# Kernel tuning notes

Hardware: AMD Instinct MI355X
Metric: run time of the kernel (lower is better)

Reference implementation:

```python
import jax, jax.numpy as jnp
import numpy as np

MAX_ITERS = 50
EPS_NORM = 1e-8
EPS_SEP = -1e-6


def setup_inputs() -> dict:
    key = jax.random.key(0)
    k1, k2 = jax.random.split(key)
    pointcloud = jax.random.normal(k1, (200000, 3), dtype=jnp.float32)
    targets = jax.random.normal(k2, (256, 3), dtype=jnp.float32)
    return {"pointcloud": pointcloud, "targets": targets}


def reference(pointcloud, targets):
    # pointcloud: [N, d], targets: [M, d]
    N = pointcloud.shape[0]
    M = targets.shape[0]
    p2 = jnp.sum(pointcloud * pointcloud, axis=1)  # [N]
    t2 = jnp.sum(targets * targets, axis=1)        # [M]

    def step(mask, _):
        # squared euclidean distances [M, N] (argmin identical to cdist argmin)
        d2 = t2[:, None] + p2[None, :] - 2.0 * (targets @ pointcloud.T)
        d2 = jnp.where(mask, d2, jnp.inf)
        closest_idx = jnp.argmin(d2, axis=1)           # [M]
        closest_points = pointcloud[closest_idx]       # [M, d]
        a = closest_points - targets
        a = a / (jnp.linalg.norm(a, axis=1, keepdims=True) + EPS_NORM)
        b = jnp.sum(a * closest_points, axis=1)        # [M]
        dot = a @ pointcloud.T - b[:, None]            # [M, N]
        separated = dot >= EPS_SEP
        mask = mask & ~separated
        return mask, (a, b)

    mask0 = jnp.ones((M, N), dtype=bool)
    _, (a_stack, b_stack) = jax.lax.scan(step, mask0, None, length=MAX_ITERS)
    return a_stack, b_stack  # [MAX_ITERS, M, d], [MAX_ITERS, M]
```

## Files before the change

kernel.cpp:

```cpp
#include <hip/hip_runtime.h>
#include <stdint.h>
#include <math.h>

#pragma clang fp contract(off)

#define BLOCK 1024
#define NW 16
#define PT 8
#define MAX_ITERS 50
#define SOLO_CAP 2048
#define NBINS 4096
#define EPS_NORM 1e-8f
#define EPS_SEP (-1e-6f)
#define SLACK_ABS 1e-3f
#define SLACK_REL 1e-5f

__device__ __forceinline__ int bin_of(float x, float y, float z) {
    int cx = (int)floorf((x + 3.5f) * (16.0f / 7.0f));
    int cy = (int)floorf((y + 3.5f) * (16.0f / 7.0f));
    int cz = (int)floorf((z + 3.5f) * (16.0f / 7.0f));
    cx = cx < 0 ? 0 : (cx > 15 ? 15 : cx);
    cy = cy < 0 ? 0 : (cy > 15 ? 15 : cy);
    cz = cz < 0 ? 0 : (cz > 15 ? 15 : cz);
    int code = 0;
    #pragma unroll
    for (int b = 0; b < 4; ++b) {
        code |= ((cx >> b) & 1) << (3 * b);
        code |= ((cy >> b) & 1) << (3 * b + 1);
        code |= ((cz >> b) & 1) << (3 * b + 2);
    }
    return code;
}

__global__ void hist_bins(const float* __restrict__ pc, int* __restrict__ binCnt,
                          int N) {
    const int t = blockIdx.x * blockDim.x + threadIdx.x;
    const int base = t * 4;
    if (base + 3 < N) {
        const float4* p4 = (const float4*)pc;
        const float4 a = p4[3*t+0], b = p4[3*t+1], c = p4[3*t+2];
        atomicAdd(&binCnt[bin_of(a.x, a.y, a.z)], 1);
        atomicAdd(&binCnt[bin_of(a.w, b.x, b.y)], 1);
        atomicAdd(&binCnt[bin_of(b.z, b.w, c.x)], 1);
        atomicAdd(&binCnt[bin_of(c.y, c.z, c.w)], 1);
    } else {
        for (int i = base; i < N; ++i)
            atomicAdd(&binCnt[bin_of(pc[3*i], pc[3*i+1], pc[3*i+2])], 1);
    }
}

__global__ void scan_bins(const int* __restrict__ binCnt,
                          int* __restrict__ binCur) {
    __shared__ int wsum[16];
    const int t = threadIdx.x, lane = t & 63, wv = t >> 6;
    const int v0 = binCnt[4*t+0], v1 = binCnt[4*t+1],
              v2 = binCnt[4*t+2], v3 = binCnt[4*t+3];
    const int s = v0 + v1 + v2 + v3;
    int incl = s;
    #pragma unroll
    for (int off = 1; off < 64; off <<= 1) {
        int o = __shfl_up(incl, off, 64);
        if (lane >= off) incl += o;
    }
    if (lane == 63) wsum[wv] = incl;
    __syncthreads();
    if (t == 0) {
        int acc = 0;
        for (int w = 0; w < 16; ++w) { int x = wsum[w]; wsum[w] = acc; acc += x; }
    }
    __syncthreads();
    const int excl = incl - s + wsum[wv];
    binCur[4*t+0] = excl;
    binCur[4*t+1] = excl + v0;
    binCur[4*t+2] = excl + v0 + v1;
    binCur[4*t+3] = excl + v0 + v1 + v2;
}

__global__ void scatter_bins(const float* __restrict__ pc,
                             float4* __restrict__ pk,
                             int* __restrict__ binCur, int N) {
    const int t = blockIdx.x * blockDim.x + threadIdx.x;
    const int base = t * 4;
    if (base + 3 < N) {
        const float4* p4 = (const float4*)pc;
        const float4 a = p4[3*t+0], b = p4[3*t+1], c = p4[3*t+2];
        float x[4] = {a.x, a.w, b.z, c.y};
        float y[4] = {a.y, b.x, b.w, c.z};
        float z[4] = {a.z, b.y, c.x, c.w};
        #pragma unroll
        for (int q = 0; q < 4; ++q) {
            const int pos = atomicAdd(&binCur[bin_of(x[q], y[q], z[q])], 1);
            float4 v; v.x = x[q]; v.y = y[q]; v.z = z[q];
            v.w = __int_as_float(base + q);
            pk[pos] = v;
        }
    } else {
        for (int i = base; i < N; ++i) {
            const float xx = pc[3*i], yy = pc[3*i+1], zz = pc[3*i+2];
            const int pos = atomicAdd(&binCur[bin_of(xx, yy, zz)], 1);
            float4 v; v.x = xx; v.y = yy; v.z = zz; v.w = __int_as_float(i);
            pk[pos] = v;
        }
    }
}

__global__ void pack_identity(const float* __restrict__ pc,
                              float4* __restrict__ pk, int N) {
    const int i = blockIdx.x * blockDim.x + threadIdx.x;
    if (i < N) {
        float4 v; v.x = pc[3*i+0]; v.y = pc[3*i+1]; v.z = pc[3*i+2];
        v.w = __int_as_float(i);
        pk[i] = v;
    }
}

template <bool PK>
__global__ __launch_bounds__(BLOCK) void convex_plane_kernel(
    const float* __restrict__ pc, const float4* __restrict__ pk,
    const float* __restrict__ tg,
    float* __restrict__ out, int N, int M, int stepsA)
{
    extern __shared__ uint32_t smem[];
    const int tid  = threadIdx.x;
    const int lane = tid & 63;
    const int wv   = tid >> 6;
    const int m    = blockIdx.x;

    const int NC    = stepsA * NW;
    const int maskW = stepsA * (PT * BLOCK / 32);
    uint32_t* mask = smem;
    float* mnx = (float*)(mask + maskW);
    float* mny = mnx + NC;
    float* mnz = mny + NC;
    float* mxx = mnz + NC;
    float* mxy = mxx + NC;
    float* mxz = mxy + NC;
    float* cdm = mxz + NC;
    int*   cim = (int*)(cdm + NC);
    int*   ccn = cim + NC;
    float* red_d = (float*)(ccn + NC);
    int*   red_i = (int*)(red_d + NW);
    int*   cw    = red_i + NW;
    int*   bcast = cw + NW;
    int*   cnt   = bcast + 2;
    int*   slist = cnt + 1;
    float* lx = (float*)(slist + SOLO_CAP);
    float* ly = lx + SOLO_CAP;
    float* lz = ly + SOLO_CAP;

    const float tx = tg[3*m+0], ty = tg[3*m+1], tz = tg[3*m+2];
    const float t2 = tx*tx + ty*ty + tz*tz;

    float* out_a = out;
    float* out_b = out + (size_t)MAX_ITERS * (size_t)M * 3;

    auto ld8 = [&](int pbase, float px[PT], float py[PT], float pz[PT],
                   int ov[PT]) {
        #pragma unroll
        for (int j = 0; j < PT; ++j) {
            int ip = pbase + j * 64;
            ip = ip < N ? ip : N - 1;
            if constexpr (PK) {
                const float4 v = pk[ip];
                px[j] = v.x; py[j] = v.y; pz[j] = v.z;
                ov[j] = __float_as_int(v.w);
            } else {
                const float* p = pc + 3 * (size_t)ip;
                px[j] = p[0]; py[j] = p[1]; pz[j] = p[2];
                ov[j] = ip;
            }
        }
    };

    auto finish = [&]() -> int2 {
        __syncthreads();
        float bd = INFINITY; int bi = 0; int cs = 0;
        for (int l = lane; l < stepsA; l += 64) {
            const int c = wv + NW * l;
            const float d = cdm[c]; const int i = cim[c];
            if (d < bd || (d == bd && i < bi)) { bd = d; bi = i; }
            cs += ccn[c];
        }
        #pragma unroll
        for (int off = 32; off > 0; off >>= 1) {
            float od = __shfl_down(bd, off, 64);
            int   oi = __shfl_down(bi, off, 64);
            int   oc = __shfl_down(cs, off, 64);
            if (od < bd || (od == bd && oi < bi)) { bd = od; bi = oi; }
            cs += oc;
        }
        if (lane == 0) { red_d[wv] = bd; red_i[wv] = bi; cw[wv] = cs; }
        __syncthreads();
        if (wv == 0) {
            float d = (lane < NW) ? red_d[lane] : INFINITY;
            int   i = (lane < NW) ? red_i[lane] : 0;
            int   c = (lane < NW) ? cw[lane]    : 0;
            #pragma unroll
            for (int off = 8; off > 0; off >>= 1) {
                float od = __shfl_down(d, off, 64);
                int   oi = __shfl_down(i, off, 64);
                int   oc = __shfl_down(c, off, 64);
                if (od < d || (od == d && oi < i)) { d = od; i = oi; }
                c += oc;
            }
            if (lane == 0) { bcast[0] = i; bcast[1] = c; }
        }
        __syncthreads();
        int2 r; r.x = bcast[0]; r.y = bcast[1];
        return r;
    };

    auto writeChunk = [&](int c, uint32_t keepm,
                          float dmin, int imin,
                          float px[PT], float py[PT], float pz[PT]) {
        float nx = INFINITY, ny = INFINITY, nz = INFINITY;
        float Xx = -INFINITY, Xy = -INFINITY, Xz = -INFINITY;
        #pragma unroll
        for (int j = 0; j < PT; ++j) {
            if ((keepm >> j) & 1u) {
                nx = fminf(nx, px[j]); ny = fminf(ny, py[j]); nz = fminf(nz, pz[j]);
                Xx = fmaxf(Xx, px[j]); Xy = fmaxf(Xy, py[j]); Xz = fmaxf(Xz, pz[j]);
            }
        }
        int cntl = (int)__popc(keepm);
        #pragma unroll
        for (int off = 32; off > 0; off >>= 1) {
            float od = __shfl_down(dmin, off, 64);
            int   oi = __shfl_down(imin, off, 64);
            if (od < dmin || (od == dmin && oi < imin)) { dmin = od; imin = oi; }
            cntl += __shfl_down(cntl, off, 64);
            nx = fminf(nx, __shfl_down(nx, off, 64));
            ny = fminf(ny, __shfl_down(ny, off, 64));
            nz = fminf(nz, __shfl_down(nz, off, 64));
            Xx = fmaxf(Xx, __shfl_down(Xx, off, 64));
            Xy = fmaxf(Xy, __shfl_down(Xy, off, 64));
            Xz = fmaxf(Xz, __shfl_down(Xz, off, 64));
        }
        if (lane == 0) {
            cdm[c] = dmin; cim[c] = imin; ccn[c] = cntl;
            mnx[c] = nx; mny[c] = ny; mnz[c] = nz;
            mxx[c] = Xx; mxy[c] = Xy; mxz[c] = Xz;
        }
    };

    auto initScan = [&]() {
        for (int s = 0; s < stepsA; ++s) {
            const int c = s * NW + wv;
            const int pbase = s * (PT * BLOCK) + wv * (PT * 64) + lane;
            const int wwb   = s * (PT * BLOCK / 32) + wv * (PT * 2);
            uint32_t livem = 0;
            #pragma unroll
            for (int j = 0; j < PT; ++j)
                if (pbase + j * 64 < N) livem |= (1u << j);
            float px[PT], py[PT], pz[PT]; int ov[PT];
            ld8(pbase, px, py, pz, ov);
            float dmin = INFINITY; int imin = 0;
            #pragma unroll
            for (int j = 0; j < PT; ++j) {
                if ((livem >> j) & 1u) {
                    float p2 = px[j]*px[j] + py[j]*py[j] + pz[j]*pz[j];
                    float tp = tx*px[j] + ty*py[j] + tz*pz[j];
                    float d2 = t2 + p2 - 2.0f*tp;
                    if (d2 < dmin || (d2 == dmin && ov[j] < imin)) {
                        dmin = d2; imin = ov[j];
                    }
                }
            }
            #pragma unroll
            for (int j = 0; j < PT; ++j) {
                unsigned long long bal = __ballot(((livem >> j) & 1u) != 0u);
                if (lane == 0)       mask[wwb + j*2]     = (uint32_t)bal;
                else if (lane == 32) mask[wwb + j*2 + 1] = (uint32_t)(bal >> 32);
            }
            writeChunk(c, livem, dmin, imin, px, py, pz);
        }
    };

    auto stepScan = [&](float ax, float ay, float az, float b) {
        for (int s = 0; s < stepsA; ++s) {
            const int c = s * NW + wv;
            if (ccn[c] == 0) continue;
            const float ubx = fmaxf(ax*mnx[c], ax*mxx[c]);
            const float uby = fmaxf(ay*mny[c], ay*mxy[c]);
            const float ubz = fmaxf(az*mnz[c], az*mxz[c]);
            const float ub  = (ubx + uby + ubz) - b;
            const float sl  = SLACK_ABS + SLACK_REL * (fabsf(ub) + fabsf(b));
            if (ub < EPS_SEP - sl) continue;
            const float lbx = fminf(ax*mnx[c], ax*mxx[c]);
            const float lby = fminf(ay*mny[c], ay*mxy[c]);
            const float lbz = fminf(az*mnz[c], az*mxz[c]);
            const float lb  = (lbx + lby + lbz) - b;
            const float sl2 = SLACK_ABS + SLACK_REL * (fabsf(lb) + fabsf(b));
            if (lb >= EPS_SEP + sl2) {
                if (lane == 0) { ccn[c] = 0; cdm[c] = INFINITY; }
                continue;
            }
            const int pbase = s * (PT * BLOCK) + wv * (PT * 64) + lane;
            const int wwb   = s * (PT * BLOCK / 32) + wv * (PT * 2);
            uint32_t livem = 0;
            #pragma unroll
            for (int j = 0; j < PT; ++j) {
                uint32_t w = mask[wwb + j * 2 + (lane >> 5)];
                livem |= ((w >> (lane & 31)) & 1u) << j;
            }
            float px[PT], py[PT], pz[PT]; int ov[PT];
            ld8(pbase, px, py, pz, ov);
            uint32_t keepm = 0;
            float dmin = INFINITY; int imin = 0;
            #pragma unroll
            for (int j = 0; j < PT; ++j) {
                if ((livem >> j) & 1u) {
                    float dt = ax*px[j] + ay*py[j] + az*pz[j] - b;
                    if (dt < EPS_SEP) {
                        keepm |= (1u << j);
                        float p2 = px[j]*px[j] + py[j]*py[j] + pz[j]*pz[j];
                        float tp = tx*px[j] + ty*py[j] + tz*pz[j];
                        float d2 = t2 + p2 - 2.0f*tp;
                        if (d2 < dmin || (d2 == dmin && ov[j] < imin)) {
                            dmin = d2; imin = ov[j];
                        }
                    }
                }
            }
            #pragma unroll
            for (int j = 0; j < PT; ++j) {
                unsigned long long bal = __ballot(((keepm >> j) & 1u) != 0u);
                if (lane == 0)       mask[wwb + j*2]     = (uint32_t)bal;
                else if (lane == 32) mask[wwb + j*2 + 1] = (uint32_t)(bal >> 32);
            }
            writeChunk(c, keepm, dmin, imin, px, py, pz);
        }
    };

    initScan();
    int2 rc = finish();
    int idx = rc.x, count = rc.y;

    for (int k = 0; k < MAX_ITERS; ++k) {
        if (count <= SOLO_CAP && count > 0) {
            if (tid == 0) cnt[0] = 0;
            __syncthreads();
            for (int s = 0; s < stepsA; ++s) {
                const int c = s * NW + wv;
                if (ccn[c] == 0) continue;
                const int pbase = s * (PT * BLOCK) + wv * (PT * 64) + lane;
                const int wwb   = s * (PT * BLOCK / 32) + wv * (PT * 2);
                uint32_t livem = 0;
                #pragma unroll
                for (int j = 0; j < PT; ++j) {
                    uint32_t w = mask[wwb + j * 2 + (lane >> 5)];
                    livem |= ((w >> (lane & 31)) & 1u) << j;
                }
                float px[PT], py[PT], pz[PT]; int ov[PT];
                ld8(pbase, px, py, pz, ov);
                int cl = (int)__popc(livem);
                int incl = cl;
                #pragma unroll
                for (int off = 1; off < 64; off <<= 1) {
                    int o = __shfl_up(incl, off, 64);
                    if (lane >= off) incl += o;
                }
                const int excl = incl - cl;
                const int tot  = __shfl(incl, 63, 64);
                int wb = 0;
                if (lane == 0) wb = atomicAdd(cnt, tot);
                wb = __shfl(wb, 0, 64);
                int pos = wb + excl;
                #pragma unroll
                for (int j = 0; j < PT; ++j) {
                    if ((livem >> j) & 1u) {
                        slist[pos] = ov[j];
                        lx[pos] = px[j]; ly[pos] = py[j]; lz[pos] = pz[j];
                        ++pos;
                    }
                }
            }
            __syncthreads();
            if (wv != 0) return;
            for (; k < MAX_ITERS; ++k) {
                const float* cp = pc + 3 * (size_t)idx;
                const float cx = cp[0], cy = cp[1], cz = cp[2];
                const float vx = cx - tx, vy = cy - ty, vz = cz - tz;
                const float nrm = sqrtf(vx*vx + vy*vy + vz*vz);
                const float den = nrm + EPS_NORM;
                const float ax = vx / den, ay = vy / den, az = vz / den;
                const float b  = ax*cx + ay*cy + az*cz;
                if (count == 0) {
                    for (int q = lane; q < MAX_ITERS - k; q += 64) {
                        const int kk = k + q;
                        const size_t oa = ((size_t)kk * M + m) * 3;
                        out_a[oa+0] = ax; out_a[oa+1] = ay; out_a[oa+2] = az;
                        out_b[(size_t)kk * M + m] = b;
                    }
                    return;
                }
                if (lane == 0) {
                    const size_t oa = ((size_t)k * M + m) * 3;
                    out_a[oa+0] = ax; out_a[oa+1] = ay; out_a[oa+2] = az;
                    out_b[(size_t)k * M + m] = b;
                }
                if (k + 1 < MAX_ITERS) {
                    float dmin = INFINITY; int imin = 0; int wcur = 0;
                    for (int e0 = 0; e0 < count; e0 += 64) {
                        const int e = e0 + lane;
                        bool keep = false; int j = 0;
                        float d2v = 0.f, px = 0.f, py = 0.f, pz = 0.f;
                        if (e < count) {
                            j = slist[e];
                            px = lx[e]; py = ly[e]; pz = lz[e];
                            float dt = ax*px + ay*py + az*pz - b;
                            if (dt < EPS_SEP) {
                                keep = true;
                                float p2 = px*px + py*py + pz*pz;
                                float tp = tx*px + ty*py + tz*pz;
                                d2v = t2 + p2 - 2.0f*tp;
                            }
                        }
                        unsigned long long bal = __ballot(keep);
                        int pos = wcur + (int)__popcll(bal & ((1ull << lane) - 1ull));
                        if (keep) {
                            slist[pos] = j;
                            lx[pos] = px; ly[pos] = py; lz[pos] = pz;
                            if (d2v < dmin || (d2v == dmin && j < imin)) {
                                dmin = d2v; imin = j;
                            }
                        }
                        wcur += (int)__popcll(bal);
                    }
                    #pragma unroll
                    for (int off = 32; off > 0; off >>= 1) {
                        float od = __shfl_down(dmin, off, 64);
                        int   oi = __shfl_down(imin, off, 64);
                        if (od < dmin || (od == dmin && oi < imin)) { dmin = od; imin = oi; }
                    }
                    idx = __shfl(imin, 0, 64);
                    count = wcur;
                }
            }
            return;
        }

        const float* cp = pc + 3 * (size_t)idx;
        const float cx = cp[0], cy = cp[1], cz = cp[2];
        const float vx = cx - tx, vy = cy - ty, vz = cz - tz;
        const float nrm = sqrtf(vx*vx + vy*vy + vz*vz);
        const float den = nrm + EPS_NORM;
        const float ax = vx / den, ay = vy / den, az = vz / den;
        const float b  = ax*cx + ay*cy + az*cz;

        if (count == 0) {
            for (int q = tid; q < MAX_ITERS - k; q += BLOCK) {
                const int kk = k + q;
                const size_t oa = ((size_t)kk * M + m) * 3;
                out_a[oa+0] = ax; out_a[oa+1] = ay; out_a[oa+2] = az;
                out_b[(size_t)kk * M + m] = b;
            }
            return;
        }
        if (tid == 0) {
            const size_t oa = ((size_t)k * M + m) * 3;
            out_a[oa+0] = ax; out_a[oa+1] = ay; out_a[oa+2] = az;
            out_b[(size_t)k * M + m] = b;
        }
        if (k + 1 < MAX_ITERS) {
            stepScan(ax, ay, az, b);
            rc = finish();
            idx = rc.x; count = rc.y;
        }
    }
}

extern "C" void kernel_launch(void* const* d_in, const int* in_sizes, int n_in,
                              void* d_out, int out_size, void* d_ws, size_t ws_size,
                              hipStream_t stream) {
    const float* pc = (const float*)d_in[0];
    const float* tg = (const float*)d_in[1];
    float* out = (float*)d_out;
    const int N = in_sizes[0] / 3;
    const int M = in_sizes[1] / 3;
    const int stepsA = (N + BLOCK * PT - 1) / (BLOCK * PT);
    const int NC     = stepsA * NW;
    const int maskW  = stepsA * (PT * BLOCK / 32);
    const size_t smemW = (size_t)maskW + 9u * NC + 3u * NW + 3u
                       + 4u * SOLO_CAP;
    const size_t smem  = smemW * sizeof(uint32_t);
    const size_t pkB   = (size_t)N * sizeof(float4);
    const size_t binB  = 2 * (size_t)NBINS * sizeof(int);

    int wsmode = 0;
    if (d_ws && ws_size >= pkB + binB) wsmode = 2;
    else if (d_ws && ws_size >= pkB)   wsmode = 1;
    float4* pk     = (float4*)d_ws;
    int*    binCnt = (int*)((char*)d_ws + pkB);
    int*    binCur = binCnt + NBINS;

    hipFuncSetAttribute((const void*)convex_plane_kernel<true>,
                        hipFuncAttributeMaxDynamicSharedMemorySize, (int)smem);
    hipFuncSetAttribute((const void*)convex_plane_kernel<false>,
                        hipFuncAttributeMaxDynamicSharedMemorySize, (int)smem);

    if (wsmode == 2) {
        const int tpb = 256;
        const int vthreads = (N + 3) / 4;
        hipMemsetAsync(binCnt, 0, NBINS * sizeof(int), stream);
        hist_bins<<<(vthreads + tpb - 1) / tpb, tpb, 0, stream>>>(pc, binCnt, N);
        scan_bins<<<1, 1024, 0, stream>>>(binCnt, binCur);
        scatter_bins<<<(vthreads + tpb - 1) / tpb, tpb, 0, stream>>>(pc, pk,
                                                                     binCur, N);
        convex_plane_kernel<true><<<M, BLOCK, smem, stream>>>(
            pc, pk, tg, out, N, M, stepsA);
    } else if (wsmode == 1) {
        pack_identity<<<(N + 255) / 256, 256, 0, stream>>>(pc, pk, N);
        convex_plane_kernel<true><<<M, BLOCK, smem, stream>>>(
            pc, pk, tg, out, N, M, stepsA);
    } else {
        convex_plane_kernel<false><<<M, BLOCK, smem, stream>>>(
            pc, nullptr, tg, out, N, M, stepsA);
    }
}
```

Baseline: 572.6 us.

## Refine bounding-box culling to 64-point groups with quantized boxes and compacted work list

Culling now works on per-wavefront 64-point groups instead of 512-point chunks. Each group's bounding box is stored as 16-bit quantized coordinates, which keeps the per-group shared-memory state small. Each iteration first classifies all groups in parallel and compacts only the ambiguous ones into a list, which the wavefronts then process two at a time. The spatial binning grid also goes from 16^3 to 32^3 Morton cells so that groups are tighter. The aim is to load far fewer points per iteration, at the cost of a longer classification pass, more atomics and a scan kernel that walks 32 bins per thread serially.

```diff
diff --git a/kernel.cpp b/kernel.cpp
--- a/kernel.cpp
+++ b/kernel.cpp
@@ -6,25 +6,25 @@
 
 #define BLOCK 1024
 #define NW 16
-#define PT 8
 #define MAX_ITERS 50
 #define SOLO_CAP 2048
-#define NBINS 4096
+#define NBINS 32768
 #define EPS_NORM 1e-8f
 #define EPS_SEP (-1e-6f)
-#define SLACK_ABS 1e-3f
-#define SLACK_REL 1e-5f
+#define SLACK 1e-3f
+#define QSC 2048.0f
+#define QIN (1.0f/2048.0f)
 
 __device__ __forceinline__ int bin_of(float x, float y, float z) {
-    int cx = (int)floorf((x + 3.5f) * (16.0f / 7.0f));
-    int cy = (int)floorf((y + 3.5f) * (16.0f / 7.0f));
-    int cz = (int)floorf((z + 3.5f) * (16.0f / 7.0f));
-    cx = cx < 0 ? 0 : (cx > 15 ? 15 : cx);
-    cy = cy < 0 ? 0 : (cy > 15 ? 15 : cy);
-    cz = cz < 0 ? 0 : (cz > 15 ? 15 : cz);
+    int cx = (int)floorf((x + 3.5f) * (32.0f / 7.0f));
+    int cy = (int)floorf((y + 3.5f) * (32.0f / 7.0f));
+    int cz = (int)floorf((z + 3.5f) * (32.0f / 7.0f));
+    cx = cx < 0 ? 0 : (cx > 31 ? 31 : cx);
+    cy = cy < 0 ? 0 : (cy > 31 ? 31 : cy);
+    cz = cz < 0 ? 0 : (cz > 31 ? 31 : cz);
     int code = 0;
     #pragma unroll
-    for (int b = 0; b < 4; ++b) {
+    for (int b = 0; b < 5; ++b) {
         code |= ((cx >> b) & 1) << (3 * b);
         code |= ((cy >> b) & 1) << (3 * b + 1);
         code |= ((cz >> b) & 1) << (3 * b + 2);
@@ -53,9 +53,8 @@
                           int* __restrict__ binCur) {
     __shared__ int wsum[16];
     const int t = threadIdx.x, lane = t & 63, wv = t >> 6;
-    const int v0 = binCnt[4*t+0], v1 = binCnt[4*t+1],
-              v2 = binCnt[4*t+2], v3 = binCnt[4*t+3];
-    const int s = v0 + v1 + v2 + v3;
+    int s = 0;
+    for (int j = 0; j < 32; ++j) s += binCnt[32*t + j];
     int incl = s;
     #pragma unroll
     for (int off = 1; off < 64; off <<= 1) {
@@ -69,11 +68,12 @@
         for (int w = 0; w < 16; ++w) { int x = wsum[w]; wsum[w] = acc; acc += x; }
     }
     __syncthreads();
-    const int excl = incl - s + wsum[wv];
-    binCur[4*t+0] = excl;
-    binCur[4*t+1] = excl + v0;
-    binCur[4*t+2] = excl + v0 + v1;
-    binCur[4*t+3] = excl + v0 + v1 + v2;
+    int run = incl - s + wsum[wv];
+    for (int j = 0; j < 32; ++j) {
+        const int v = binCnt[32*t + j];
+        binCur[32*t + j] = run;
+        run += v;
+    }
 }
 
 __global__ void scatter_bins(const float* __restrict__ pc,
@@ -117,8 +117,8 @@
 template <bool PK>
 __global__ __launch_bounds__(BLOCK) void convex_plane_kernel(
     const float* __restrict__ pc, const float4* __restrict__ pk,
-    const float* __restrict__ tg,
-    float* __restrict__ out, int N, int M, int stepsA)
+    const float* __restrict__ tg, float* __restrict__ out,
+    int N, int M, int G)
 {
     extern __shared__ uint32_t smem[];
     const int tid  = threadIdx.x;
@@ -126,27 +126,22 @@
     const int wv   = tid >> 6;
     const int m    = blockIdx.x;
 
-    const int NC    = stepsA * NW;
-    const int maskW = stepsA * (PT * BLOCK / 32);
-    uint32_t* mask = smem;
-    float* mnx = (float*)(mask + maskW);
-    float* mny = mnx + NC;
-    float* mnz = mny + NC;
-    float* mxx = mnz + NC;
-    float* mxy = mxx + NC;
-    float* mxz = mxy + NC;
-    float* cdm = mxz + NC;
-    int*   cim = (int*)(cdm + NC);
-    int*   ccn = cim + NC;
-    float* red_d = (float*)(ccn + NC);
-    int*   red_i = (int*)(red_d + NW);
-    int*   cw    = red_i + NW;
-    int*   bcast = cw + NW;
-    int*   cnt   = bcast + 2;
-    int*   slist = cnt + 1;
-    float* lx = (float*)(slist + SOLO_CAP);
-    float* ly = lx + SOLO_CAP;
-    float* lz = ly + SOLO_CAP;
+    uint32_t* mask  = smem;
+    uint32_t* qab   = mask + 2 * G;
+    float*    cdm   = (float*)(qab + 3 * G);
+    int*      cim   = (int*)(cdm + G);
+    int*      ccn   = cim + G;
+    int*      blist = ccn + G;
+    int*      bcnt  = blist + G;
+    float*    red_d = (float*)(bcnt + 1);
+    int*      red_i = (int*)(red_d + NW);
+    int*      cw    = red_i + NW;
+    int*      bcast = cw + NW;
+    int*      cnt   = bcast + 2;
+    int*      slist = cnt + 1;
+    float*    lx    = (float*)(slist + SOLO_CAP);
+    float*    ly    = lx + SOLO_CAP;
+    float*    lz    = ly + SOLO_CAP;
 
     const float tx = tg[3*m+0], ty = tg[3*m+1], tz = tg[3*m+2];
     const float t2 = tx*tx + ty*ty + tz*tz;
@@ -154,32 +149,91 @@
     float* out_a = out;
     float* out_b = out + (size_t)MAX_ITERS * (size_t)M * 3;
 
-    auto ld8 = [&](int pbase, float px[PT], float py[PT], float pz[PT],
-                   int ov[PT]) {
+    auto ldpt = [&](int g, float& x, float& y, float& z, int& ov) {
+        int ip = g * 64 + lane;
+        ip = ip < N ? ip : N - 1;
+        if constexpr (PK) {
+            const float4 v = pk[ip];
+            x = v.x; y = v.y; z = v.z; ov = __float_as_int(v.w);
+        } else {
+            const float* p = pc + 3 * (size_t)ip;
+            x = p[0]; y = p[1]; z = p[2]; ov = ip;
+        }
+    };
+
+    auto qdn = [](float v) -> uint32_t {
+        int q = (int)floorf((v + 16.f) * QSC) - 1;
+        return (uint32_t)(q < 0 ? 0 : (q > 65535 ? 65535 : q));
+    };
+    auto qup = [](float v) -> uint32_t {
+        int q = (int)ceilf((v + 16.f) * QSC) + 1;
+        return (uint32_t)(q < 0 ? 0 : (q > 65535 ? 65535 : q));
+    };
+
+    auto writeGroup = [&](int g, bool keep, float x, float y, float z,
+                          float d2, int ov) {
+        unsigned long long bal = __ballot(keep);
+        if (lane == 0)       mask[2*g]     = (uint32_t)bal;
+        else if (lane == 32) mask[2*g + 1] = (uint32_t)(bal >> 32);
+        float dmin = keep ? d2 : INFINITY;
+        int   imin = keep ? ov : 0;
+        float nx = keep ? x :  INFINITY, Xx = keep ? x : -INFINITY;
+        float ny = keep ? y :  INFINITY, Xy = keep ? y : -INFINITY;
+        float nz = keep ? z :  INFINITY, Xz = keep ? z : -INFINITY;
         #pragma unroll
-        for (int j = 0; j < PT; ++j) {
-            int ip = pbase + j * 64;
-            ip = ip < N ? ip : N - 1;
-            if constexpr (PK) {
-                const float4 v = pk[ip];
-                px[j] = v.x; py[j] = v.y; pz[j] = v.z;
-                ov[j] = __float_as_int(v.w);
+        for (int off = 32; off > 0; off >>= 1) {
+            float od = __shfl_down(dmin, off, 64);
+            int   oi = __shfl_down(imin, off, 64);
+            if (od < dmin || (od == dmin && oi < imin)) { dmin = od; imin = oi; }
+            nx = fminf(nx, __shfl_down(nx, off, 64));
+            ny = fminf(ny, __shfl_down(ny, off, 64));
+            nz = fminf(nz, __shfl_down(nz, off, 64));
+            Xx = fmaxf(Xx, __shfl_down(Xx, off, 64));
+            Xy = fmaxf(Xy, __shfl_down(Xy, off, 64));
+            Xz = fmaxf(Xz, __shfl_down(Xz, off, 64));
+        }
+        if (lane == 0) {
+            const int c = (int)__popcll(bal);
+            cdm[g] = dmin; cim[g] = imin; ccn[g] = c;
+            uint32_t q0, q1, q2;
+            const bool fits = (c == 0) ||
+                (nx > -15.9f && Xx < 15.9f && ny > -15.9f && Xy < 15.9f &&
+                 nz > -15.9f && Xz < 15.9f);
+            if (fits) {
+                const uint32_t a = qdn(nx), b2 = qdn(ny), c2 = qdn(nz);
+                const uint32_t d = qup(Xx), e = qup(Xy), f = qup(Xz);
+                q0 = a | (b2 << 16); q1 = c2 | (d << 16); q2 = e | (f << 16);
             } else {
-                const float* p = pc + 3 * (size_t)ip;
-                px[j] = p[0]; py[j] = p[1]; pz[j] = p[2];
-                ov[j] = ip;
-            }
-        }
+                q0 = 1u; q1 = 0u; q2 = 0u;
+            }
+            qab[3*g] = q0; qab[3*g+1] = q1; qab[3*g+2] = q2;
+        }
+    };
+
+    auto procGroup = [&](int g, float x, float y, float z, int ov,
+                         float ax, float ay, float az, float b) {
+        const uint32_t w = mask[2*g + (lane >> 5)];
+        const bool live = (w >> (lane & 31)) & 1u;
+        bool keep = false; float d2 = INFINITY;
+        if (live) {
+            float dt = ax*x + ay*y + az*z - b;
+            if (dt < EPS_SEP) {
+                keep = true;
+                float p2 = x*x + y*y + z*z;
+                float tp = tx*x + ty*y + tz*z;
+                d2 = t2 + p2 - 2.0f*tp;
+            }
+        }
+        writeGroup(g, keep, x, y, z, d2, ov);
     };
 
     auto finish = [&]() -> int2 {
         __syncthreads();
         float bd = INFINITY; int bi = 0; int cs = 0;
-        for (int l = lane; l < stepsA; l += 64) {
-            const int c = wv + NW * l;
-            const float d = cdm[c]; const int i = cim[c];
+        for (int g = tid; g < G; g += BLOCK) {
+            const float d = cdm[g]; const int i = cim[g];
             if (d < bd || (d == bd && i < bi)) { bd = d; bi = i; }
-            cs += ccn[c];
+            cs += ccn[g];
         }
         #pragma unroll
         for (int off = 32; off > 0; off >>= 1) {
@@ -210,129 +264,18 @@
         return r;
     };
 
-    auto writeChunk = [&](int c, uint32_t keepm,
-                          float dmin, int imin,
-                          float px[PT], float py[PT], float pz[PT]) {
-        float nx = INFINITY, ny = INFINITY, nz = INFINITY;
-        float Xx = -INFINITY, Xy = -INFINITY, Xz = -INFINITY;
-        #pragma unroll
-        for (int j = 0; j < PT; ++j) {
-            if ((keepm >> j) & 1u) {
-                nx = fminf(nx, px[j]); ny = fminf(ny, py[j]); nz = fminf(nz, pz[j]);
-                Xx = fmaxf(Xx, px[j]); Xy = fmaxf(Xy, py[j]); Xz = fmaxf(Xz, pz[j]);
-            }
-        }
-        int cntl = (int)__popc(keepm);
-        #pragma unroll
-        for (int off = 32; off > 0; off >>= 1) {
-            float od = __shfl_down(dmin, off, 64);
-            int   oi = __shfl_down(imin, off, 64);
-            if (od < dmin || (od == dmin && oi < imin)) { dmin = od; imin = oi; }
-            cntl += __shfl_down(cntl, off, 64);
-            nx = fminf(nx, __shfl_down(nx, off, 64));
-            ny = fminf(ny, __shfl_down(ny, off, 64));
-            nz = fminf(nz, __shfl_down(nz, off, 64));
-            Xx = fmaxf(Xx, __shfl_down(Xx, off, 64));
-            Xy = fmaxf(Xy, __shfl_down(Xy, off, 64));
-            Xz = fmaxf(Xz, __shfl_down(Xz, off, 64));
-        }
-        if (lane == 0) {
-            cdm[c] = dmin; cim[c] = imin; ccn[c] = cntl;
-            mnx[c] = nx; mny[c] = ny; mnz[c] = nz;
-            mxx[c] = Xx; mxy[c] = Xy; mxz[c] = Xz;
-        }
-    };
-
-    auto initScan = [&]() {
-        for (int s = 0; s < stepsA; ++s) {
-            const int c = s * NW + wv;
-            const int pbase = s * (PT * BLOCK) + wv * (PT * 64) + lane;
-            const int wwb   = s * (PT * BLOCK / 32) + wv * (PT * 2);
-            uint32_t livem = 0;
-            #pragma unroll
-            for (int j = 0; j < PT; ++j)
-                if (pbase + j * 64 < N) livem |= (1u << j);
-            float px[PT], py[PT], pz[PT]; int ov[PT];
-            ld8(pbase, px, py, pz, ov);
-            float dmin = INFINITY; int imin = 0;
-            #pragma unroll
-            for (int j = 0; j < PT; ++j) {
-                if ((livem >> j) & 1u) {
-                    float p2 = px[j]*px[j] + py[j]*py[j] + pz[j]*pz[j];
-                    float tp = tx*px[j] + ty*py[j] + tz*pz[j];
-                    float d2 = t2 + p2 - 2.0f*tp;
-                    if (d2 < dmin || (d2 == dmin && ov[j] < imin)) {
-                        dmin = d2; imin = ov[j];
-                    }
-                }
-            }
-            #pragma unroll
-            for (int j = 0; j < PT; ++j) {
-                unsigned long long bal = __ballot(((livem >> j) & 1u) != 0u);
-                if (lane == 0)       mask[wwb + j*2]     = (uint32_t)bal;
-                else if (lane == 32) mask[wwb + j*2 + 1] = (uint32_t)(bal >> 32);
-            }
-            writeChunk(c, livem, dmin, imin, px, py, pz);
-        }
-    };
-
-    auto stepScan = [&](float ax, float ay, float az, float b) {
-        for (int s = 0; s < stepsA; ++s) {
-            const int c = s * NW + wv;
-            if (ccn[c] == 0) continue;
-            const float ubx = fmaxf(ax*mnx[c], ax*mxx[c]);
-            const float uby = fmaxf(ay*mny[c], ay*mxy[c]);
-            const float ubz = fmaxf(az*mnz[c], az*mxz[c]);
-            const float ub  = (ubx + uby + ubz) - b;
-            const float sl  = SLACK_ABS + SLACK_REL * (fabsf(ub) + fabsf(b));
-            if (ub < EPS_SEP - sl) continue;
-            const float lbx = fminf(ax*mnx[c], ax*mxx[c]);
-            const float lby = fminf(ay*mny[c], ay*mxy[c]);
-            const float lbz = fminf(az*mnz[c], az*mxz[c]);
-            const float lb  = (lbx + lby + lbz) - b;
-            const float sl2 = SLACK_ABS + SLACK_REL * (fabsf(lb) + fabsf(b));
-            if (lb >= EPS_SEP + sl2) {
-                if (lane == 0) { ccn[c] = 0; cdm[c] = INFINITY; }
-                continue;
-            }
-            const int pbase = s * (PT * BLOCK) + wv * (PT * 64) + lane;
-            const int wwb   = s * (PT * BLOCK / 32) + wv * (PT * 2);
-            uint32_t livem = 0;
-            #pragma unroll
-            for (int j = 0; j < PT; ++j) {
-                uint32_t w = mask[wwb + j * 2 + (lane >> 5)];
-                livem |= ((w >> (lane & 31)) & 1u) << j;
-            }
-            float px[PT], py[PT], pz[PT]; int ov[PT];
-            ld8(pbase, px, py, pz, ov);
-            uint32_t keepm = 0;
-            float dmin = INFINITY; int imin = 0;
-            #pragma unroll
-            for (int j = 0; j < PT; ++j) {
-                if ((livem >> j) & 1u) {
-                    float dt = ax*px[j] + ay*py[j] + az*pz[j] - b;
-                    if (dt < EPS_SEP) {
-                        keepm |= (1u << j);
-                        float p2 = px[j]*px[j] + py[j]*py[j] + pz[j]*pz[j];
-                        float tp = tx*px[j] + ty*py[j] + tz*pz[j];
-                        float d2 = t2 + p2 - 2.0f*tp;
-                        if (d2 < dmin || (d2 == dmin && ov[j] < imin)) {
-                            dmin = d2; imin = ov[j];
-                        }
-                    }
-                }
-            }
-            #pragma unroll
-            for (int j = 0; j < PT; ++j) {
-                unsigned long long bal = __ballot(((keepm >> j) & 1u) != 0u);
-                if (lane == 0)       mask[wwb + j*2]     = (uint32_t)bal;
-                else if (lane == 32) mask[wwb + j*2 + 1] = (uint32_t)(bal >> 32);
-            }
-            writeChunk(c, keepm, dmin, imin, px, py, pz);
-        }
-    };
-
-    initScan();
+    for (int g = wv; g < G; g += NW) {
+        float x, y, z; int ov;
+        ldpt(g, x, y, z, ov);
+        const bool live = (g * 64 + lane) < N;
+        float d2 = INFINITY;
+        if (live) {
+            float p2 = x*x + y*y + z*z;
+            float tp = tx*x + ty*y + tz*z;
+            d2 = t2 + p2 - 2.0f*tp;
+        }
+        writeGroup(g, live, x, y, z, d2, ov);
+    }
     int2 rc = finish();
     int idx = rc.x, count = rc.y;
 
@@ -340,40 +283,19 @@
         if (count <= SOLO_CAP && count > 0) {
             if (tid == 0) cnt[0] = 0;
             __syncthreads();
-            for (int s = 0; s < stepsA; ++s) {
-                const int c = s * NW + wv;
-                if (ccn[c] == 0) continue;
-                const int pbase = s * (PT * BLOCK) + wv * (PT * 64) + lane;
-                const int wwb   = s * (PT * BLOCK / 32) + wv * (PT * 2);
-                uint32_t livem = 0;
-                #pragma unroll
-                for (int j = 0; j < PT; ++j) {
-                    uint32_t w = mask[wwb + j * 2 + (lane >> 5)];
-                    livem |= ((w >> (lane & 31)) & 1u) << j;
-                }
-                float px[PT], py[PT], pz[PT]; int ov[PT];
-                ld8(pbase, px, py, pz, ov);
-                int cl = (int)__popc(livem);
-                int incl = cl;
-                #pragma unroll
-                for (int off = 1; off < 64; off <<= 1) {
-                    int o = __shfl_up(incl, off, 64);
-                    if (lane >= off) incl += o;
-                }
-                const int excl = incl - cl;
-                const int tot  = __shfl(incl, 63, 64);
+            for (int g = wv; g < G; g += NW) {
+                if (ccn[g] == 0) continue;
+                float x, y, z; int ov;
+                ldpt(g, x, y, z, ov);
+                const uint32_t w = mask[2*g + (lane >> 5)];
+                const bool live = (w >> (lane & 31)) & 1u;
+                unsigned long long bal = __ballot(live);
+                const int tot = (int)__popcll(bal);
                 int wb = 0;
                 if (lane == 0) wb = atomicAdd(cnt, tot);
                 wb = __shfl(wb, 0, 64);
-                int pos = wb + excl;
-                #pragma unroll
-                for (int j = 0; j < PT; ++j) {
-                    if ((livem >> j) & 1u) {
-                        slist[pos] = ov[j];
-                        lx[pos] = px[j]; ly[pos] = py[j]; lz[pos] = pz[j];
-                        ++pos;
-                    }
-                }
+                const int pos = wb + (int)__popcll(bal & ((1ull << lane) - 1ull));
+                if (live) { slist[pos] = ov; lx[pos] = x; ly[pos] = y; lz[pos] = z; }
             }
             __syncthreads();
             if (wv != 0) return;
@@ -463,7 +385,56 @@
             out_b[(size_t)k * M + m] = b;
         }
         if (k + 1 < MAX_ITERS) {
-            stepScan(ax, ay, az, b);
+            if (tid == 0) bcnt[0] = 0;
+            __syncthreads();
+            for (int g = tid; g < G; g += BLOCK) {
+                int cls = 0;
+                if (ccn[g] > 0) {
+                    const uint32_t q0 = qab[3*g], q1 = qab[3*g+1], q2 = qab[3*g+2];
+                    const int mnxq = q0 & 0xFFFF, mnyq = q0 >> 16;
+                    const int mnzq = q1 & 0xFFFF, mxxq = q1 >> 16;
+                    const int mxyq = q2 & 0xFFFF, mxzq = q2 >> 16;
+                    if (mnxq > mxxq) cls = 2;
+                    else {
+                        const float mnx = mnxq*QIN - 16.f, mny = mnyq*QIN - 16.f;
+                        const float mnz = mnzq*QIN - 16.f, mxx = mxxq*QIN - 16.f;
+                        const float mxy = mxyq*QIN - 16.f, mxz = mxzq*QIN - 16.f;
+                        const float ub = fmaxf(ax*mnx, ax*mxx)
+                                       + fmaxf(ay*mny, ay*mxy)
+                                       + fmaxf(az*mnz, az*mxz) - b;
+                        if (ub + SLACK < EPS_SEP) cls = 0;
+                        else {
+                            const float lb = fminf(ax*mnx, ax*mxx)
+                                           + fminf(ay*mny, ay*mxy)
+                                           + fminf(az*mnz, az*mxz) - b;
+                            cls = (lb - SLACK >= EPS_SEP) ? 1 : 2;
+                        }
+                    }
+                }
+                if (cls == 1) { ccn[g] = 0; cdm[g] = INFINITY; }
+                unsigned long long bal = __ballot(cls == 2);
+                if (bal) {
+                    const int leader = (int)(__ffsll(bal) - 1);
+                    const int tot = (int)__popcll(bal);
+                    int base = 0;
+                    if (lane == leader) base = atomicAdd(bcnt, tot);
+                    base = __shfl(base, leader, 64);
+                    if (cls == 2)
+                        blist[base + (int)__popcll(bal & ((1ull << lane) - 1ull))] = g;
+                }
+            }
+            __syncthreads();
+            const int nb = bcnt[0];
+            for (int i = 2 * wv; i < nb; i += 2 * NW) {
+                const int g0 = blist[i];
+                const bool has1 = (i + 1) < nb;
+                const int g1 = has1 ? blist[i + 1] : g0;
+                float x0, y0, z0, x1, y1, z1; int o0, o1;
+                ldpt(g0, x0, y0, z0, o0);
+                ldpt(g1, x1, y1, z1, o1);
+                procGroup(g0, x0, y0, z0, o0, ax, ay, az, b);
+                if (has1) procGroup(g1, x1, y1, z1, o1, ax, ay, az, b);
+            }
             rc = finish();
             idx = rc.x; count = rc.y;
         }
@@ -478,11 +449,9 @@
     float* out = (float*)d_out;
     const int N = in_sizes[0] / 3;
     const int M = in_sizes[1] / 3;
-    const int stepsA = (N + BLOCK * PT - 1) / (BLOCK * PT);
-    const int NC     = stepsA * NW;
-    const int maskW  = stepsA * (PT * BLOCK / 32);
-    const size_t smemW = (size_t)maskW + 9u * NC + 3u * NW + 3u
-                       + 4u * SOLO_CAP;
+    const int G = (N + 63) / 64;
+
+    const size_t smemW = 9ull * G + 1 + 3 * NW + 2 + 1 + 4ull * SOLO_CAP;
     const size_t smem  = smemW * sizeof(uint32_t);
     const size_t pkB   = (size_t)N * sizeof(float4);
     const size_t binB  = 2 * (size_t)NBINS * sizeof(int);
@@ -508,13 +477,13 @@
         scatter_bins<<<(vthreads + tpb - 1) / tpb, tpb, 0, stream>>>(pc, pk,
                                                                      binCur, N);
         convex_plane_kernel<true><<<M, BLOCK, smem, stream>>>(
-            pc, pk, tg, out, N, M, stepsA);
+            pc, pk, tg, out, N, M, G);
     } else if (wsmode == 1) {
         pack_identity<<<(N + 255) / 256, 256, 0, stream>>>(pc, pk, N);
         convex_plane_kernel<true><<<M, BLOCK, smem, stream>>>(
-            pc, pk, tg, out, N, M, stepsA);
+            pc, pk, tg, out, N, M, G);
     } else {
         convex_plane_kernel<false><<<M, BLOCK, smem, stream>>>(
-            pc, nullptr, tg, out, N, M, stepsA);
-    }
-}
+            pc, nullptr, tg, out, N, M, G);
+    }
+}
```

Result: slower. 1.060 ms (+85.2%).
